# Optimization experiments

Measured on AMD Instinct MI355X. Metric: run time of the kernel, lower is better.

The kernel has to match this reference:

```python
import jax, jax.numpy as jnp
import numpy as np

N_NODES = 50000
N_EDGES = 500000
IN_CH = 256
HID = 64
HEADS = 8
OUT_CH = 16
NEG_SLOPE = 0.2  # PyG GATConv default


def setup_inputs() -> dict:
    key = jax.random.key(0)
    ks = jax.random.split(key, 10)
    x = jax.random.normal(ks[0], (N_NODES, IN_CH), dtype=jnp.float32)
    edge_index = jax.random.randint(ks[1], (2, N_EDGES), 0, N_NODES, dtype=jnp.int64)
    s1 = 1.0 / np.sqrt(IN_CH)
    W1 = jax.random.uniform(ks[2], (IN_CH, HEADS * HID), jnp.float32, -s1, s1)
    att_src1 = jax.random.normal(ks[3], (HEADS, HID), dtype=jnp.float32) * 0.1
    att_dst1 = jax.random.normal(ks[4], (HEADS, HID), dtype=jnp.float32) * 0.1
    b1 = jnp.zeros((HEADS * HID,), jnp.float32)
    s2 = 1.0 / np.sqrt(HEADS * HID)
    W2 = jax.random.uniform(ks[5], (HEADS * HID, OUT_CH), jnp.float32, -s2, s2)
    att_src2 = jax.random.normal(ks[6], (1, OUT_CH), dtype=jnp.float32) * 0.1
    att_dst2 = jax.random.normal(ks[7], (1, OUT_CH), dtype=jnp.float32) * 0.1
    b2 = jnp.zeros((OUT_CH,), jnp.float32)
    return {"x": x, "edge_index": edge_index, "W1": W1, "att_src1": att_src1,
            "att_dst1": att_dst1, "b1": b1, "W2": W2, "att_src2": att_src2,
            "att_dst2": att_dst2, "b2": b2}


def _gat_conv(x, src, dst, W, att_src, att_dst, bias, heads, out_ch, concat, n_nodes):
    # Linear transform: [N, H, C]
    h = (x @ W).reshape(n_nodes, heads, out_ch)
    # Per-node attention logits: [N, H]
    a_src = jnp.einsum('nhc,hc->nh', h, att_src)
    a_dst = jnp.einsum('nhc,hc->nh', h, att_dst)
    # Edge-wise attention score (message src -> dst): [E, H]
    e = jax.nn.leaky_relu(a_src[src] + a_dst[dst], NEG_SLOPE)
    # Segment softmax over incoming edges of each destination node
    emax = jax.ops.segment_max(e, dst, num_segments=n_nodes)  # [N, H]
    emax = jnp.where(jnp.isfinite(emax), emax, 0.0)
    e = jnp.exp(e - emax[dst])
    denom = jax.ops.segment_sum(e, dst, num_segments=n_nodes)  # [N, H]
    alpha = e / (denom[dst] + 1e-16)
    # Weighted scatter-add aggregation: [N, H, C]
    msg = h[src] * alpha[:, :, None]
    out = jax.ops.segment_sum(msg, dst, num_segments=n_nodes)
    if concat:
        out = out.reshape(n_nodes, heads * out_ch)
    else:
        out = out.mean(axis=1)
    return out + bias


def reference(x, edge_index, W1, att_src1, att_dst1, b1, W2, att_src2, att_dst2, b2):
    n = x.shape[0]
    # PyG GATConv adds self-loops by default
    loops = jnp.arange(n, dtype=edge_index.dtype)
    src = jnp.concatenate([edge_index[0], loops])
    dst = jnp.concatenate([edge_index[1], loops])
    # dropout (p=0.6) is identity in eval mode
    h = _gat_conv(x, src, dst, W1, att_src1, att_dst1, b1, HEADS, HID, True, n)
    h = jax.nn.elu(h)
    out = _gat_conv(h, src, dst, W2, att_src2, att_dst2, b2, 1, OUT_CH, False, n)
    return jax.nn.log_softmax(out, axis=1)
```

## Files before the change

kernel.cpp:

```cpp
#include <hip/hip_runtime.h>
#include <math.h>

#define N_NODES 50000
#define N_EDGES 500000
#define IN_CH 256
#define D1 512
#define HEADS 8
#define HID 64
#define OUT_CH 16
#define NEG_SLOPE 0.2f

typedef __bf16 bf16x8 __attribute__((ext_vector_type(8)));
typedef float f32x4 __attribute__((ext_vector_type(4)));
typedef float f32x2 __attribute__((ext_vector_type(2)));

__device__ inline void fp8x8_to_f32(uint2 u, float* f) {
    f32x2 p0 = __builtin_amdgcn_cvt_pk_f32_fp8(u.x, false);
    f32x2 p1 = __builtin_amdgcn_cvt_pk_f32_fp8(u.x, true);
    f32x2 p2 = __builtin_amdgcn_cvt_pk_f32_fp8(u.y, false);
    f32x2 p3 = __builtin_amdgcn_cvt_pk_f32_fp8(u.y, true);
    f[0] = p0.x; f[1] = p0.y; f[2] = p1.x; f[3] = p1.y;
    f[4] = p2.x; f[5] = p2.y; f[6] = p3.x; f[7] = p3.y;
}

__device__ inline void fp8x16_to_f32(uint4 u, float* f) {
    fp8x8_to_f32(make_uint2(u.x, u.y), f);
    fp8x8_to_f32(make_uint2(u.z, u.w), f + 8);
}

__device__ inline unsigned char f32_to_fp8(float v) {
    return (unsigned char)(__builtin_amdgcn_cvt_pk_fp8_f32(v, v, 0, false) & 0xff);
}

__device__ inline float leaky_exp(float e) {
    float v = e > 0.f ? e : NEG_SLOPE * e;
    return __expf(v);
}

__device__ inline void gl_lds16(const __bf16* g, __bf16* l) {
    __builtin_amdgcn_global_load_lds(
        (const __attribute__((address_space(1))) unsigned int*)g,
        (__attribute__((address_space(3))) unsigned int*)l,
        16, 0, 0);
}

__device__ inline bf16x8 f32x8_to_bf16x8(const float4& a, const float4& b) {
    bf16x8 r;
    r[0] = (__bf16)a.x; r[1] = (__bf16)a.y; r[2] = (__bf16)a.z; r[3] = (__bf16)a.w;
    r[4] = (__bf16)b.x; r[5] = (__bf16)b.y; r[6] = (__bf16)b.z; r[7] = (__bf16)b.w;
    return r;
}

__global__ __launch_bounds__(256) void k_prep(const float* __restrict__ W1,
                                              const float* __restrict__ W2,
                                              const int* __restrict__ edst,
                                              __bf16* __restrict__ Wt,
                                              __bf16* __restrict__ Wt2,
                                              int* __restrict__ deg) {
    int t = blockIdx.x * 256 + threadIdx.x;
    int nthr = gridDim.x * 256;
    for (int i = t; i < D1 * IN_CH; i += nthr) {
        int n = i >> 8, k = i & 255;
        Wt[i] = (__bf16)W1[k * D1 + n];
    }
    for (int i = t; i < D1 * OUT_CH; i += nthr) {
        int n = i >> 9, k = i & 511;
        Wt2[i] = (__bf16)W2[k * OUT_CH + n];
    }
    for (int i = t; i < N_EDGES; i += nthr) atomicAdd(&deg[edst[i]], 1);
}

__global__ __launch_bounds__(512) void k_gemm1d(const float* __restrict__ X,
                                                const __bf16* __restrict__ Wt,
                                                const float* __restrict__ att_src,
                                                const float* __restrict__ att_dst,
                                                unsigned char* __restrict__ Hf8,
                                                float* __restrict__ a_src1,
                                                float* __restrict__ a_dst1) {
    __shared__ __align__(16) __bf16 Bs[256 * 64];
    int tid = threadIdx.x;
    int wid = tid >> 6, lane = tid & 63;
    int lq = lane >> 4, lm = lane & 15;
    int half = blockIdx.x & 1;
    int rowt = blockIdx.x >> 1;
    int row0 = rowt * 128 + wid * 16;
    int c0 = half * 256;
    int arow = row0 + lm;
    if (arow >= N_NODES) arow = N_NODES - 1;
    const float* ap = X + (size_t)arow * IN_CH;
    int sw = lm & 7;
    f32x4 acc[16] = {};
    #pragma unroll
    for (int s = 0; s < 4; ++s) {
        if (s) __syncthreads();
        #pragma unroll
        for (int it = 0; it < 4; ++it) {
            int idx = it * 512 + tid;
            int r = idx >> 3;
            int p = idx & 7;
            gl_lds16(&Wt[(size_t)(c0 + r) * IN_CH + s * 64 + ((p ^ (r & 7)) * 8)],
                     &Bs[idx * 8]);
        }
        float4 a00 = *(const float4*)&ap[s * 64 + lq * 8];
        float4 a01 = *(const float4*)&ap[s * 64 + lq * 8 + 4];
        float4 a10 = *(const float4*)&ap[s * 64 + 32 + lq * 8];
        float4 a11 = *(const float4*)&ap[s * 64 + 32 + lq * 8 + 4];
        bf16x8 af0 = f32x8_to_bf16x8(a00, a01);
        bf16x8 af1 = f32x8_to_bf16x8(a10, a11);
        __syncthreads();
        #pragma unroll
        for (int kt = 0; kt < 2; ++kt) {
            bf16x8 af = kt ? af1 : af0;
            #pragma unroll
            for (int c = 0; c < 16; ++c) {
                bf16x8 bfr = *(const bf16x8*)&Bs[(c * 16 + lm) * 64 +
                                                 (((kt * 4 + lq) ^ sw) * 8)];
                acc[c] = __builtin_amdgcn_mfma_f32_16x16x32_bf16(af, bfr, acc[c], 0, 0, 0);
            }
        }
    }
    float as_v[16], ad_v[16];
    #pragma unroll
    for (int c = 0; c < 16; ++c) {
        int h = half * 4 + (c >> 2);
        as_v[c] = att_src[h * HID + (c & 3) * 16 + lm];
        ad_v[c] = att_dst[h * HID + (c & 3) * 16 + lm];
    }
    #pragma unroll
    for (int r = 0; r < 4; ++r) {
        int gr = row0 + lq * 4 + r;
        bool ok = gr < N_NODES;
        #pragma unroll
        for (int h = 0; h < 4; ++h) {
            float ps = 0.f, pd = 0.f;
            #pragma unroll
            for (int cc = 0; cc < 4; ++cc) {
                int c = h * 4 + cc;
                float v = acc[c][r];
                ps += v * as_v[c];
                pd += v * ad_v[c];
                if (ok)
                    Hf8[(size_t)gr * D1 + c0 + c * 16 + lm] = f32_to_fp8(v);
            }
            #pragma unroll
            for (int off = 1; off < 16; off <<= 1) {
                ps += __shfl_xor(ps, off);
                pd += __shfl_xor(pd, off);
            }
            if (lm == 0 && ok) {
                a_src1[gr * HEADS + half * 4 + h] = ps;
                a_dst1[gr * HEADS + half * 4 + h] = pd;
            }
        }
    }
}

__global__ __launch_bounds__(1024) void k_scan1(const int* __restrict__ deg,
                                                int* __restrict__ offsets,
                                                int* __restrict__ bsum) {
    __shared__ int wsum[16];
    int tid = threadIdx.x, lane = tid & 63, wid = tid >> 6;
    int i = blockIdx.x * 1024 + tid;
    int v = (i < N_NODES) ? deg[i] : 0;
    int x = v;
    #pragma unroll
    for (int off = 1; off < 64; off <<= 1) {
        int t = __shfl_up(x, off);
        if (lane >= off) x += t;
    }
    if (lane == 63) wsum[wid] = x;
    __syncthreads();
    if (wid == 0) {
        int s = (lane < 16) ? wsum[lane] : 0;
        #pragma unroll
        for (int off = 1; off < 16; off <<= 1) {
            int t = __shfl_up(s, off);
            if (lane >= off) s += t;
        }
        if (lane < 16) wsum[lane] = s;
    }
    __syncthreads();
    int wbase = wid ? wsum[wid - 1] : 0;
    if (i < N_NODES) offsets[i] = wbase + x - v;
    if (tid == 1023) bsum[blockIdx.x] = wsum[15];
}

__global__ __launch_bounds__(256) void k_scan3(int* __restrict__ offsets,
                                               const int* __restrict__ bsum,
                                               int* __restrict__ cursor) {
    __shared__ int bpre_s[64];
    int tid = threadIdx.x;
    const int nb = (N_NODES + 1023) / 1024;
    if (tid < 64) {
        int v = (tid < nb) ? bsum[tid] : 0;
        int x = v;
        #pragma unroll
        for (int off = 1; off < 64; off <<= 1) {
            int t = __shfl_up(x, off);
            if (tid >= off) x += t;
        }
        bpre_s[tid] = x - v;
        if (blockIdx.x == 0 && tid == nb - 1) offsets[N_NODES] = x;
    }
    __syncthreads();
    int i = blockIdx.x * 256 + tid;
    if (i < N_NODES) {
        int o = offsets[i] + bpre_s[i >> 10];
        offsets[i] = o;
        cursor[i] = o;
    }
}

__global__ void k_scatter(const int* __restrict__ esrc, const int* __restrict__ edst,
                          int* __restrict__ cursor, int* __restrict__ csr) {
    int e = blockIdx.x * blockDim.x + threadIdx.x;
    if (e >= N_EDGES) return;
    int s = esrc[e], d = edst[e];
    int pos = atomicAdd(&cursor[d], 1);
    csr[pos] = s;
}

__device__ inline void agg1_pair(const unsigned char* __restrict__ Hf8,
                                 const float* __restrict__ a_src,
                                 int sA, int sB, int chb, int head, float ad_h,
                                 float* o, float& lsum) {
    uint4 uA = *(const uint4*)&Hf8[(size_t)sA * D1 + chb];
    uint4 uB = *(const uint4*)&Hf8[(size_t)sB * D1 + chb];
    float wA = leaky_exp(a_src[sA * HEADS + head] + ad_h);
    float wB = leaky_exp(a_src[sB * HEADS + head] + ad_h);
    float fA[16], fB[16];
    fp8x16_to_f32(uA, fA);
    fp8x16_to_f32(uB, fB);
    lsum += wA + wB;
    #pragma unroll
    for (int j = 0; j < 16; ++j) o[j] += wA * fA[j] + wB * fB[j];
}

__global__ __launch_bounds__(256) void k_agg1(const unsigned char* __restrict__ Hf8,
                                              const float* __restrict__ a_src,
                                              const float* __restrict__ a_dst,
                                              const int* __restrict__ offsets,
                                              const int* __restrict__ csr,
                                              const float* __restrict__ b1,
                                              __bf16* __restrict__ OUT) {
    int wave = (blockIdx.x * blockDim.x + threadIdx.x) >> 6;
    int lane = threadIdx.x & 63;
    if (wave >= N_NODES) return;
    int d = wave;
    int half = lane >> 5;
    int l32 = lane & 31;
    int chb = l32 * 16;
    int head = l32 >> 2;
    float ad_h = a_dst[d * HEADS + head];
    float o[16];
    #pragma unroll
    for (int j = 0; j < 16; ++j) o[j] = 0.f;
    float lsum = 0.f;
    if (half == 0) {
        float wself = leaky_exp(a_src[d * HEADS + head] + ad_h);
        uint4 hu = *(const uint4*)&Hf8[(size_t)d * D1 + chb];
        float hv[16];
        fp8x16_to_f32(hu, hv);
        lsum = wself;
        #pragma unroll
        for (int j = 0; j < 16; ++j) o[j] = wself * hv[j];
    }
    int beg = offsets[d], end = offsets[d + 1];
    int idx = beg;
    if (idx + 4 <= end) {
        int sA = csr[idx + half];
        int sB = csr[idx + 2 + half];
        for (; idx + 8 <= end; idx += 4) {
            int sA2 = csr[idx + 4 + half];
            int sB2 = csr[idx + 6 + half];
            agg1_pair(Hf8, a_src, sA, sB, chb, head, ad_h, o, lsum);
            sA = sA2; sB = sB2;
        }
        agg1_pair(Hf8, a_src, sA, sB, chb, head, ad_h, o, lsum);
        idx += 4;
    }
    for (; idx < end; idx += 2) {
        int e = idx + half;
        bool valid = e < end;
        int s = valid ? csr[e] : csr[idx];
        uint4 u = *(const uint4*)&Hf8[(size_t)s * D1 + chb];
        float w = valid ? leaky_exp(a_src[s * HEADS + head] + ad_h) : 0.f;
        float f[16];
        fp8x16_to_f32(u, f);
        lsum += w;
        #pragma unroll
        for (int j = 0; j < 16; ++j) o[j] += w * f[j];
    }
    #pragma unroll
    for (int j = 0; j < 16; ++j) o[j] += __shfl_xor(o[j], 32);
    lsum += __shfl_xor(lsum, 32);
    if (half == 0) {
        float inv = 1.0f / (lsum + 1e-16f);
        __bf16 r[16];
        #pragma unroll
        for (int j = 0; j < 16; ++j) {
            float v = o[j] * inv + b1[chb + j];
            v = v > 0.f ? v : (__expf(v) - 1.0f);
            r[j] = (__bf16)v;
        }
        *(uint4*)&OUT[(size_t)d * D1 + chb]     = *(uint4*)&r[0];
        *(uint4*)&OUT[(size_t)d * D1 + chb + 8] = *(uint4*)&r[8];
    }
}

__global__ __launch_bounds__(256) void k_gemm2_mfma(const __bf16* __restrict__ A,
                                                    const __bf16* __restrict__ Wt2,
                                                    const float* __restrict__ as2v,
                                                    const float* __restrict__ ad2v,
                                                    __bf16* __restrict__ H2,
                                                    float* __restrict__ a_src2,
                                                    float* __restrict__ a_dst2) {
    int tid = threadIdx.x;
    int wid = tid >> 6, lane = tid & 63;
    int lq = lane >> 4, lm = lane & 15;
    int row0 = blockIdx.x * 64 + wid * 16;
    int arow = row0 + lm;
    const __bf16* ap = A + (size_t)(arow < N_NODES ? arow : 0) * D1;
    f32x4 acc = {};
    #pragma unroll
    for (int k0 = 0; k0 < 16; ++k0) {
        bf16x8 af  = *(const bf16x8*)&ap[k0 * 32 + lq * 8];
        bf16x8 bfr = *(const bf16x8*)&Wt2[lm * D1 + k0 * 32 + lq * 8];
        acc = __builtin_amdgcn_mfma_f32_16x16x32_bf16(af, bfr, acc, 0, 0, 0);
    }
    float as_c = as2v[lm], ad_c = ad2v[lm];
    #pragma unroll
    for (int r = 0; r < 4; ++r) {
        int gr = row0 + lq * 4 + r;
        float v = acc[r];
        if (gr < N_NODES) H2[gr * OUT_CH + lm] = (__bf16)v;
        float ps = v * as_c, pd = v * ad_c;
        #pragma unroll
        for (int off = 1; off < 16; off <<= 1) {
            ps += __shfl_xor(ps, off);
            pd += __shfl_xor(pd, off);
        }
        if (lm == 0 && gr < N_NODES) { a_src2[gr] = ps; a_dst2[gr] = pd; }
    }
}

__device__ inline void agg2_pair(const __bf16* __restrict__ H2,
                                 const float* __restrict__ a_src,
                                 int s0, int s1, int c, float ad,
                                 float& o, float& lsum) {
    float h0 = (float)H2[s0 * OUT_CH + c];
    float h1 = (float)H2[s1 * OUT_CH + c];
    float wt0 = leaky_exp(a_src[s0] + ad);
    float wt1 = leaky_exp(a_src[s1] + ad);
    lsum += wt0 + wt1;
    o += wt0 * h0 + wt1 * h1;
}

__global__ __launch_bounds__(256) void k_agg2(const __bf16* __restrict__ H2,
                                              const float* __restrict__ a_src,
                                              const float* __restrict__ a_dst,
                                              const int* __restrict__ offsets,
                                              const int* __restrict__ csr,
                                              const float* __restrict__ b2,
                                              float* __restrict__ OUT) {
    int wave = (blockIdx.x * blockDim.x + threadIdx.x) >> 6;
    int lane = threadIdx.x & 63;
    if (wave >= N_NODES) return;
    int d = wave;
    int g = lane >> 4, c = lane & 15;
    float ad = a_dst[d];
    float o = 0.f, lsum = 0.f;
    if (g == 0) {
        float wself = leaky_exp(a_src[d] + ad);
        o = wself * (float)H2[d * OUT_CH + c];
        lsum = wself;
    }
    int beg = offsets[d], end = offsets[d + 1];
    int i0 = beg + g;
    if (i0 + 4 < end) {
        int s0 = csr[i0], s1 = csr[i0 + 4];
        for (; i0 + 12 < end; i0 += 8) {
            int t0 = csr[i0 + 8], t1 = csr[i0 + 12];
            agg2_pair(H2, a_src, s0, s1, c, ad, o, lsum);
            s0 = t0; s1 = t1;
        }
        agg2_pair(H2, a_src, s0, s1, c, ad, o, lsum);
        i0 += 8;
    }
    for (; i0 < end; i0 += 4) {
        int s = csr[i0];
        float wt = leaky_exp(a_src[s] + ad);
        float h = (float)H2[s * OUT_CH + c];
        lsum += wt;
        o += wt * h;
    }
    o += __shfl_xor(o, 16);  o += __shfl_xor(o, 32);
    lsum += __shfl_xor(lsum, 16);  lsum += __shfl_xor(lsum, 32);
    float v = o / (lsum + 1e-16f) + b2[c];
    float mx = v;
    #pragma unroll
    for (int off = 1; off < 16; off <<= 1) mx = fmaxf(mx, __shfl_xor(mx, off));
    float se = __expf(v - mx);
    #pragma unroll
    for (int off = 1; off < 16; off <<= 1) se += __shfl_xor(se, off);
    float res = v - mx - logf(se);
    if (lane < 16) OUT[d * OUT_CH + lane] = res;
}

extern "C" void kernel_launch(void* const* d_in, const int* in_sizes, int n_in,
                              void* d_out, int out_size, void* d_ws, size_t ws_size,
                              hipStream_t stream) {
    const float* x        = (const float*)d_in[0];
    const int*   ei       = (const int*)d_in[1];
    const float* W1       = (const float*)d_in[2];
    const float* att_src1 = (const float*)d_in[3];
    const float* att_dst1 = (const float*)d_in[4];
    const float* b1       = (const float*)d_in[5];
    const float* W2       = (const float*)d_in[6];
    const float* att_src2 = (const float*)d_in[7];
    const float* att_dst2 = (const float*)d_in[8];
    const float* b2       = (const float*)d_in[9];
    float* out = (float*)d_out;

    const int* esrc = ei;
    const int* edst = ei + N_EDGES;

    char* ws = (char*)d_ws;
    size_t off = 0;
    auto alloc = [&](size_t bytes) { char* p = ws + off; off = (off + bytes + 255) & ~(size_t)255; return p; };
    unsigned char* Hf8 = (unsigned char*)alloc((size_t)N_NODES * D1);
    __bf16* out1   = (__bf16*)alloc((size_t)N_NODES * D1 * 2);
    __bf16* Wt     = (__bf16*)alloc((size_t)D1 * IN_CH * 2);
    __bf16* Wt2    = (__bf16*)alloc((size_t)D1 * OUT_CH * 2);
    float* a_src1  = (float*)alloc((size_t)N_NODES * HEADS * 4);
    float* a_dst1  = (float*)alloc((size_t)N_NODES * HEADS * 4);
    __bf16* h2     = (__bf16*)alloc((size_t)N_NODES * OUT_CH * 2);
    float* a_src2  = (float*)alloc((size_t)N_NODES * 4);
    float* a_dst2  = (float*)alloc((size_t)N_NODES * 4);
    int*   deg     = (int*)alloc((size_t)N_NODES * 4);
    int*   offsets = (int*)alloc((size_t)(N_NODES + 1) * 4);
    int*   cursor  = (int*)alloc((size_t)N_NODES * 4);
    int*   csr     = (int*)alloc((size_t)N_EDGES * 4);
    int*   bsum    = (int*)alloc(64 * 4);
    (void)ws_size;

    hipMemsetAsync(deg, 0, (size_t)N_NODES * 4, stream);
    k_prep<<<512, 256, 0, stream>>>(W1, W2, edst, Wt, Wt2, deg);
    int g1_blocks = ((N_NODES + 127) / 128) * 2;
    k_gemm1d<<<g1_blocks, 512, 0, stream>>>(x, Wt, att_src1, att_dst1, Hf8, a_src1, a_dst1);
    int nb = (N_NODES + 1023) / 1024;
    k_scan1<<<nb, 1024, 0, stream>>>(deg, offsets, bsum);
    k_scan3<<<(N_NODES + 255) / 256, 256, 0, stream>>>(offsets, bsum, cursor);
    k_scatter<<<(N_EDGES + 255) / 256, 256, 0, stream>>>(esrc, edst, cursor, csr);
    k_agg1<<<(N_NODES * 64 + 255) / 256, 256, 0, stream>>>(Hf8, a_src1, a_dst1, offsets, csr, b1, out1);
    k_gemm2_mfma<<<(N_NODES + 63) / 64, 256, 0, stream>>>(out1, Wt2, att_src2, att_dst2, h2, a_src2, a_dst2);
    k_agg2<<<(N_NODES * 64 + 255) / 256, 256, 0, stream>>>(h2, a_src2, a_dst2, offsets, csr, b2, out);
}
```

Before: 277.3 us.

## Fuse layer-2 linear transform and attention logits into layer-1 aggregation

Folds the second GEMM (512->16) and its attention-logit dot products into the epilogue of the layer-1 aggregation kernel. Each wave now multiplies its ELU'd 512-wide row against Wt2 with scalar FMAs and reduces with cross-lane shuffles. This removes the 50000x512 bf16 intermediate write and reread, plus one kernel launch. In exchange the MFMA matmul becomes scalar FMA work plus many shuffles inside a memory-bound gather kernel, which adds register pressure.

```diff
diff --git a/kernel.cpp b/kernel.cpp
--- a/kernel.cpp
+++ b/kernel.cpp
@@ -242,7 +242,12 @@
                                               const int* __restrict__ offsets,
                                               const int* __restrict__ csr,
                                               const float* __restrict__ b1,
-                                              __bf16* __restrict__ OUT) {
+                                              const __bf16* __restrict__ Wt2,
+                                              const float* __restrict__ as2,
+                                              const float* __restrict__ ad2,
+                                              __bf16* __restrict__ H2,
+                                              float* __restrict__ a_src2,
+                                              float* __restrict__ a_dst2) {
     int wave = (blockIdx.x * blockDim.x + threadIdx.x) >> 6;
     int lane = threadIdx.x & 63;
     if (wave >= N_NODES) return;
@@ -294,53 +299,45 @@
     #pragma unroll
     for (int j = 0; j < 16; ++j) o[j] += __shfl_xor(o[j], 32);
     lsum += __shfl_xor(lsum, 32);
-    if (half == 0) {
-        float inv = 1.0f / (lsum + 1e-16f);
-        __bf16 r[16];
-        #pragma unroll
-        for (int j = 0; j < 16; ++j) {
-            float v = o[j] * inv + b1[chb + j];
-            v = v > 0.f ? v : (__expf(v) - 1.0f);
-            r[j] = (__bf16)v;
-        }
-        *(uint4*)&OUT[(size_t)d * D1 + chb]     = *(uint4*)&r[0];
-        *(uint4*)&OUT[(size_t)d * D1 + chb + 8] = *(uint4*)&r[8];
-    }
-}
-
-__global__ __launch_bounds__(256) void k_gemm2_mfma(const __bf16* __restrict__ A,
-                                                    const __bf16* __restrict__ Wt2,
-                                                    const float* __restrict__ as2v,
-                                                    const float* __restrict__ ad2v,
-                                                    __bf16* __restrict__ H2,
-                                                    float* __restrict__ a_src2,
-                                                    float* __restrict__ a_dst2) {
-    int tid = threadIdx.x;
-    int wid = tid >> 6, lane = tid & 63;
-    int lq = lane >> 4, lm = lane & 15;
-    int row0 = blockIdx.x * 64 + wid * 16;
-    int arow = row0 + lm;
-    const __bf16* ap = A + (size_t)(arow < N_NODES ? arow : 0) * D1;
-    f32x4 acc = {};
-    #pragma unroll
-    for (int k0 = 0; k0 < 16; ++k0) {
-        bf16x8 af  = *(const bf16x8*)&ap[k0 * 32 + lq * 8];
-        bf16x8 bfr = *(const bf16x8*)&Wt2[lm * D1 + k0 * 32 + lq * 8];
-        acc = __builtin_amdgcn_mfma_f32_16x16x32_bf16(af, bfr, acc, 0, 0, 0);
-    }
-    float as_c = as2v[lm], ad_c = ad2v[lm];
-    #pragma unroll
-    for (int r = 0; r < 4; ++r) {
-        int gr = row0 + lq * 4 + r;
-        float v = acc[r];
-        if (gr < N_NODES) H2[gr * OUT_CH + lm] = (__bf16)v;
-        float ps = v * as_c, pd = v * ad_c;
-        #pragma unroll
-        for (int off = 1; off < 16; off <<= 1) {
-            ps += __shfl_xor(ps, off);
-            pd += __shfl_xor(pd, off);
-        }
-        if (lm == 0 && gr < N_NODES) { a_src2[gr] = ps; a_dst2[gr] = pd; }
+    float inv = 1.0f / (lsum + 1e-16f);
+    #pragma unroll
+    for (int j = 0; j < 16; ++j) {
+        float t = o[j] * inv + b1[chb + j];
+        o[j] = t > 0.f ? t : (__expf(t) - 1.0f);
+    }
+    int cbase = half * 8;
+    float p[8];
+    #pragma unroll
+    for (int c = 0; c < 8; ++c) {
+        const __bf16* wrow = &Wt2[(size_t)(cbase + c) * D1 + chb];
+        bf16x8 w0 = *(const bf16x8*)&wrow[0];
+        bf16x8 w1 = *(const bf16x8*)&wrow[8];
+        float acc = 0.f;
+        #pragma unroll
+        for (int j = 0; j < 8; ++j) acc += o[j] * (float)w0[j];
+        #pragma unroll
+        for (int j = 0; j < 8; ++j) acc += o[8 + j] * (float)w1[j];
+        p[c] = acc;
+    }
+    #pragma unroll
+    for (int off = 1; off < 32; off <<= 1) {
+        #pragma unroll
+        for (int c = 0; c < 8; ++c) p[c] += __shfl_xor(p[c], off);
+    }
+    float asp = 0.f, adp = 0.f;
+    #pragma unroll
+    for (int c = 0; c < 8; ++c) {
+        asp += p[c] * as2[cbase + c];
+        adp += p[c] * ad2[cbase + c];
+    }
+    asp += __shfl_xor(asp, 32);
+    adp += __shfl_xor(adp, 32);
+    if (l32 == 0) {
+        __bf16 hh[8];
+        #pragma unroll
+        for (int c = 0; c < 8; ++c) hh[c] = (__bf16)p[c];
+        *(uint4*)&H2[(size_t)d * OUT_CH + cbase] = *(uint4*)hh;
+        if (half == 0) { a_src2[d] = asp; a_dst2[d] = adp; }
     }
 }
 
@@ -429,7 +426,6 @@
     size_t off = 0;
     auto alloc = [&](size_t bytes) { char* p = ws + off; off = (off + bytes + 255) & ~(size_t)255; return p; };
     unsigned char* Hf8 = (unsigned char*)alloc((size_t)N_NODES * D1);
-    __bf16* out1   = (__bf16*)alloc((size_t)N_NODES * D1 * 2);
     __bf16* Wt     = (__bf16*)alloc((size_t)D1 * IN_CH * 2);
     __bf16* Wt2    = (__bf16*)alloc((size_t)D1 * OUT_CH * 2);
     float* a_src1  = (float*)alloc((size_t)N_NODES * HEADS * 4);
@@ -452,7 +448,8 @@
     k_scan1<<<nb, 1024, 0, stream>>>(deg, offsets, bsum);
     k_scan3<<<(N_NODES + 255) / 256, 256, 0, stream>>>(offsets, bsum, cursor);
     k_scatter<<<(N_EDGES + 255) / 256, 256, 0, stream>>>(esrc, edst, cursor, csr);
-    k_agg1<<<(N_NODES * 64 + 255) / 256, 256, 0, stream>>>(Hf8, a_src1, a_dst1, offsets, csr, b1, out1);
-    k_gemm2_mfma<<<(N_NODES + 63) / 64, 256, 0, stream>>>(out1, Wt2, att_src2, att_dst2, h2, a_src2, a_dst2);
+    k_agg1<<<(N_NODES * 64 + 255) / 256, 256, 0, stream>>>(
+        Hf8, a_src1, a_dst1, offsets, csr, b1, Wt2, att_src2, att_dst2,
+        h2, a_src2, a_dst2);
     k_agg2<<<(N_NODES * 64 + 255) / 256, 256, 0, stream>>>(h2, a_src2, a_dst2, offsets, csr, b2, out);
 }
```

Result: slower. 302.6 us (+9.1%).
